# Kernel tuning notes

Hardware: AMD Instinct MI355X
Metric: run time of the kernel (lower is better)

## Reference

```python
import jax, jax.numpy as jnp
import numpy as np

N_NODES = 100000
N_EDGES = 1600000
IN_CH = 256
HID_CH = 128


def setup_inputs() -> dict:
    key = jax.random.key(0)
    k1, k2, k3 = jax.random.split(key, 3)
    x = jax.random.normal(k1, (N_NODES, IN_CH), dtype=jnp.float32)
    edge_index = jax.random.randint(k2, (2, N_EDGES), 0, N_NODES, dtype=jnp.int64)
    # Glorot-style init for the GCN linear weight [in, out]
    W = jax.random.normal(k3, (IN_CH, HID_CH), dtype=jnp.float32) / np.sqrt(IN_CH)
    bias = jnp.zeros((HID_CH,), dtype=jnp.float32)
    # PReLU default init 0.25, per-channel
    alpha = jnp.full((HID_CH,), 0.25, dtype=jnp.float32)
    return {"x": x, "edge_index": edge_index, "W": W, "bias": bias, "alpha": alpha}


def reference(x, edge_index, W, bias, alpha):
    # GCNConv (PyG defaults): add self loops, symmetric degree norm,
    # linear transform then scatter-add aggregation, then per-channel PReLU.
    N = x.shape[0]
    self_loops = jnp.arange(N, dtype=edge_index.dtype)
    row = jnp.concatenate([edge_index[0], self_loops])  # source j
    col = jnp.concatenate([edge_index[1], self_loops])  # target i
    # degree of destination nodes (edge_weight = 1)
    deg = jax.ops.segment_sum(jnp.ones_like(col, dtype=x.dtype), col, num_segments=N)
    dinv = jnp.where(deg > 0, jax.lax.rsqrt(deg), jnp.zeros_like(deg))
    norm = dinv[row] * dinv[col]  # [E+N]
    h = x @ W  # [N, hid] dense transform first (GCNConv order)
    msgs = h[row] * norm[:, None]  # gather + scale, [E+N, hid]
    agg = jax.ops.segment_sum(msgs, col, num_segments=N) + bias  # scatter-add
    # PReLU with per-channel alpha
    return jnp.where(agg > 0, agg, alpha * agg)
```

## Files before the change

kernel.cpp:

```cpp
#include <hip/hip_runtime.h>

#define N_NODES 100000
#define N_EDGES 1600000
#define IN_CH 256
#define HID_CH 128

#define NBUCK 196
#define NBLKC 400
#define EPB   4000
#define SCAN2_LEN (NBUCK * NBLKC)
#define SCAN2_BLOCKS ((SCAN2_LEN + 255) / 256)

typedef __attribute__((ext_vector_type(8))) short short8;
typedef __attribute__((ext_vector_type(4))) float floatx4;

static __device__ __forceinline__ unsigned short f2bf(float f) {
    unsigned int u = __float_as_uint(f);
    u += 0x7fffu + ((u >> 16) & 1u);
    return (unsigned short)(u >> 16);
}

static __device__ __forceinline__ unsigned cvt_pk_bf16(float lo, float hi) {
    unsigned r;
    asm("v_cvt_pk_bf16_f32 %0, %1, %2" : "=v"(r) : "v"(lo), "v"(hi));
    return r;
}


__global__ void hist_kernel(const int* __restrict__ dst, int* __restrict__ histT) {
    __shared__ int h[NBUCK];
    int tid = threadIdx.x, blk = blockIdx.x;
    for (int b = tid; b < NBUCK; b += 256) h[b] = 0;
    __syncthreads();
    int base = blk * EPB;
    for (int e = base + tid; e < base + EPB; e += 256)
        atomicAdd(&h[dst[e] >> 9], 1);
    __syncthreads();
    for (int b = tid; b < NBUCK; b += 256) histT[b * NBLKC + blk] = h[b];
}

__global__ void gscanA_kernel(int* __restrict__ data, int* __restrict__ partials) {
    __shared__ int ss[256];
    int tid = threadIdx.x;
    int i = blockIdx.x * 256 + tid;
    int v = (i < SCAN2_LEN) ? data[i] : 0;
    ss[tid] = v;
    __syncthreads();
    for (int off = 1; off < 256; off <<= 1) {
        int t = (tid >= off) ? ss[tid - off] : 0;
        __syncthreads();
        ss[tid] += t;
        __syncthreads();
    }
    if (i < SCAN2_LEN) data[i] = ss[tid] - v;
    if (tid == 255) partials[blockIdx.x] = ss[255];
}

__global__ void gscanB_kernel(int* __restrict__ partials) {
    __shared__ int ss[512];
    int tid = threadIdx.x;
    int v = (tid < SCAN2_BLOCKS) ? partials[tid] : 0;
    ss[tid] = v;
    __syncthreads();
    for (int off = 1; off < 512; off <<= 1) {
        int t = (tid >= off) ? ss[tid - off] : 0;
        __syncthreads();
        ss[tid] += t;
        __syncthreads();
    }
    if (tid < SCAN2_BLOCKS) partials[tid] = ss[tid] - v;
}

__global__ void gscanC_kernel(int* __restrict__ data, const int* __restrict__ partials) {
    int i = blockIdx.x * 256 + threadIdx.x;
    if (i < SCAN2_LEN) data[i] += partials[blockIdx.x];
}

__global__ void scatter_coarse_kernel(const int* __restrict__ ei,
                                      const int* __restrict__ offs,
                                      unsigned* __restrict__ bucketed) {
    __shared__ int cur[NBUCK];
    int tid = threadIdx.x, blk = blockIdx.x;
    for (int b = tid; b < NBUCK; b += 256) cur[b] = offs[b * NBLKC + blk];
    __syncthreads();
    int base = blk * EPB;
    for (int e = base + tid; e < base + EPB; e += 256) {
        int src = ei[e];
        int dst = ei[N_EDGES + e];
        int b = dst >> 9;
        int pos = atomicAdd(&cur[b], 1);
        bucketed[pos] = ((unsigned)src << 9) | (unsigned)(dst & 511);
    }
}

__global__ void fine_kernel(const unsigned* __restrict__ bucketed,
                            const int* __restrict__ offs,
                            int* __restrict__ sorted,
                            int* __restrict__ row_start,
                            float* __restrict__ dinv) {
    __shared__ int bins[512];
    __shared__ int scanbuf[512];
    int b = blockIdx.x, tid = threadIdx.x;
    int bs = offs[b * NBLKC];
    int be = (b < NBUCK - 1) ? offs[(b + 1) * NBLKC] : N_EDGES;

    bins[tid] = 0;
    __syncthreads();
    for (int k = bs + tid; k < be; k += 512)
        atomicAdd(&bins[bucketed[k] & 511u], 1);
    __syncthreads();

    int c = bins[tid];
    scanbuf[tid] = c;
    __syncthreads();
    for (int off = 1; off < 512; off <<= 1) {
        int t = (tid >= off) ? scanbuf[tid - off] : 0;
        __syncthreads();
        scanbuf[tid] += t;
        __syncthreads();
    }
    int excl = scanbuf[tid] - c;

    int node = b * 512 + tid;
    if (node <= N_NODES) row_start[node] = bs + excl;
    if (node < N_NODES) dinv[node] = rsqrtf((float)(c + 1));

    bins[tid] = bs + excl;
    __syncthreads();
    for (int k = bs + tid; k < be; k += 512) {
        unsigned p = bucketed[k];
        int pos = atomicAdd(&bins[p & 511u], 1);
        sorted[pos] = (int)(p >> 9);
    }
}


__global__ void wt_kernel(const float* __restrict__ W, unsigned short* __restrict__ Wt) {
    int i = blockIdx.x * blockDim.x + threadIdx.x;
    if (i >= IN_CH * HID_CH) return;
    int k = i >> 7;
    int c = i & 127;
    Wt[c * IN_CH + k] = f2bf(W[i]);
}


__launch_bounds__(512)
__global__ void gemm_mfma_kernel(const float* __restrict__ x,
                                 const unsigned short* __restrict__ Wt,
                                 const float* __restrict__ dinv,
                                 unsigned short* __restrict__ hp) {
    __shared__ unsigned short Bs[IN_CH * HID_CH];

    int tid = threadIdx.x;

    {
        const uint4* src = (const uint4*)Wt;
#pragma unroll
        for (int i = 0; i < 8; ++i) {
            int j = i * 512 + tid;
            unsigned lb = (unsigned)j * 16u;
            unsigned c7 = (lb >> 9) & 7u;
            unsigned db = lb ^ (c7 << 4);
            *(uint4*)((char*)Bs + db) = src[j];
        }
    }
    __syncthreads();

    int wave = tid >> 6;
    int lane = tid & 63;
    int row0 = blockIdx.x * 256 + wave * 32;
    if (row0 >= N_NODES) return;

    int m = lane & 15;
    int q = lane >> 4;

    floatx4 acc[2][8];
#pragma unroll
    for (int i = 0; i < 2; ++i)
#pragma unroll
        for (int t = 0; t < 8; ++t) acc[i][t] = (floatx4){0.f, 0.f, 0.f, 0.f};

    int r0 = row0 + m;        if (r0 >= N_NODES) r0 = N_NODES - 1;
    int r1 = row0 + 16 + m;   if (r1 >= N_NODES) r1 = N_NODES - 1;
    const float* xp0 = &x[(size_t)r0 * IN_CH + q * 8];
    const float* xp1 = &x[(size_t)r1 * IN_CH + q * 8];

    float4 aA[4], aB[4];

#define LOADA(buf, kstep)                                          \
    do {                                                           \
        const float* p0_ = xp0 + (kstep) * 32;                     \
        const float* p1_ = xp1 + (kstep) * 32;                     \
        buf[0] = *(const float4*)(p0_);                            \
        buf[1] = *(const float4*)(p0_ + 4);                        \
        buf[2] = *(const float4*)(p1_);                            \
        buf[3] = *(const float4*)(p1_ + 4);                        \
    } while (0)

#define COMPUTE(buf, kstep)                                                     \
    do {                                                                        \
        union { short8 v; unsigned u[4]; } af0_, af1_;                          \
        af0_.u[0] = cvt_pk_bf16(buf[0].x, buf[0].y);                            \
        af0_.u[1] = cvt_pk_bf16(buf[0].z, buf[0].w);                            \
        af0_.u[2] = cvt_pk_bf16(buf[1].x, buf[1].y);                            \
        af0_.u[3] = cvt_pk_bf16(buf[1].z, buf[1].w);                            \
        af1_.u[0] = cvt_pk_bf16(buf[2].x, buf[2].y);                            \
        af1_.u[1] = cvt_pk_bf16(buf[2].z, buf[2].w);                            \
        af1_.u[2] = cvt_pk_bf16(buf[3].x, buf[3].y);                            \
        af1_.u[3] = cvt_pk_bf16(buf[3].z, buf[3].w);                            \
        int kb_ = ((kstep) * 32 + q * 8) * 2;                                   \
        _Pragma("unroll")                                                       \
        for (int t = 0; t < 8; ++t) {                                           \
            int c_ = t * 16 + m;                                                \
            unsigned db_ = (unsigned)(c_ * 512 + kb_) ^ ((unsigned)(c_ & 7) << 4); \
            short8 bf_ = *(const short8*)((const char*)Bs + db_);               \
            acc[0][t] = __builtin_amdgcn_mfma_f32_16x16x32_bf16(af0_.v, bf_, acc[0][t], 0, 0, 0); \
            acc[1][t] = __builtin_amdgcn_mfma_f32_16x16x32_bf16(af1_.v, bf_, acc[1][t], 0, 0, 0); \
        }                                                                       \
    } while (0)

    LOADA(aA, 0);
#pragma unroll 1
    for (int ks = 0; ks < 8; ks += 2) {
        LOADA(aB, ks + 1);
        COMPUTE(aA, ks);
        if (ks < 6) LOADA(aA, ks + 2);
        COMPUTE(aB, ks + 1);
    }

#undef LOADA
#undef COMPUTE

#pragma unroll
    for (int tile = 0; tile < 2; ++tile) {
#pragma unroll
        for (int reg = 0; reg < 4; ++reg) {
            int grow = row0 + tile * 16 + q * 4 + reg;
            if (grow < N_NODES) {
                float di = dinv[grow];
                unsigned short* op = &hp[(size_t)grow * HID_CH + m];
#pragma unroll
                for (int tp = 0; tp < 4; ++tp) {
                    unsigned d = cvt_pk_bf16(acc[tile][2 * tp][reg] * di,
                                             acc[tile][2 * tp + 1][reg] * di);
                    op[(2 * tp) * 16]     = (unsigned short)(d & 0xffffu);
                    op[(2 * tp + 1) * 16] = (unsigned short)(d >> 16);
                }
            }
        }
    }
}


static __device__ __forceinline__ void acc_bf16x8(float* acc, uint4 u, float w) {
    acc[0] += w * __uint_as_float(u.x << 16);
    acc[1] += w * __uint_as_float(u.x & 0xffff0000u);
    acc[2] += w * __uint_as_float(u.y << 16);
    acc[3] += w * __uint_as_float(u.y & 0xffff0000u);
    acc[4] += w * __uint_as_float(u.z << 16);
    acc[5] += w * __uint_as_float(u.z & 0xffff0000u);
    acc[6] += w * __uint_as_float(u.w << 16);
    acc[7] += w * __uint_as_float(u.w & 0xffff0000u);
}

__launch_bounds__(256)
__global__ void gather_finalize_kernel(const int* __restrict__ row_start,
                                       const int* __restrict__ sorted,
                                       const float* __restrict__ dinv,
                                       const unsigned short* __restrict__ hp,
                                       const float* __restrict__ bias,
                                       const float* __restrict__ alpha,
                                       float* __restrict__ out) {
    int node = (blockIdx.x * blockDim.x + threadIdx.x) >> 6;
    int lane = threadIdx.x & 63;
    if (node >= N_NODES) return;

    int beg = row_start[node];
    int end = row_start[node + 1];
    int part = lane >> 4;
    int ch = (lane & 15) * 8;

    float di = dinv[node];
    uint4 us = *(const uint4*)&hp[(size_t)node * HID_CH + ch];

    float acc[8];
#pragma unroll
    for (int i = 0; i < 8; ++i) acc[i] = 0.f;

    for (int k = beg + part; k < end; k += 16) {
        int k1 = k + 4, k2 = k + 8, k3 = k + 12;
        int e1 = end - 1;
        int s0 = sorted[k];
        int s1 = sorted[k1 < end ? k1 : e1];
        int s2 = sorted[k2 < end ? k2 : e1];
        int s3 = sorted[k3 < end ? k3 : e1];
        uint4 u0 = *(const uint4*)&hp[(size_t)s0 * HID_CH + ch];
        uint4 u1 = *(const uint4*)&hp[(size_t)s1 * HID_CH + ch];
        uint4 u2 = *(const uint4*)&hp[(size_t)s2 * HID_CH + ch];
        uint4 u3 = *(const uint4*)&hp[(size_t)s3 * HID_CH + ch];
        float w1 = k1 < end ? 1.f : 0.f;
        float w2 = k2 < end ? 1.f : 0.f;
        float w3 = k3 < end ? 1.f : 0.f;
        acc_bf16x8(acc, u0, 1.f);
        acc_bf16x8(acc, u1, w1);
        acc_bf16x8(acc, u2, w2);
        acc_bf16x8(acc, u3, w3);
    }

#pragma unroll
    for (int i = 0; i < 8; ++i) {
        acc[i] += __shfl_xor(acc[i], 16);
        acc[i] += __shfl_xor(acc[i], 32);
    }

    if (part == 0) {
        float sf[8];
        sf[0] = __uint_as_float(us.x << 16);
        sf[1] = __uint_as_float(us.x & 0xffff0000u);
        sf[2] = __uint_as_float(us.y << 16);
        sf[3] = __uint_as_float(us.y & 0xffff0000u);
        sf[4] = __uint_as_float(us.z << 16);
        sf[5] = __uint_as_float(us.z & 0xffff0000u);
        sf[6] = __uint_as_float(us.w << 16);
        sf[7] = __uint_as_float(us.w & 0xffff0000u);

        float4 b0 = *(const float4*)&bias[ch];
        float4 b1 = *(const float4*)&bias[ch + 4];
        float4 a0 = *(const float4*)&alpha[ch];
        float4 a1 = *(const float4*)&alpha[ch + 4];
        float bv[8] = {b0.x, b0.y, b0.z, b0.w, b1.x, b1.y, b1.z, b1.w};
        float av[8] = {a0.x, a0.y, a0.z, a0.w, a1.x, a1.y, a1.z, a1.w};

        float r[8];
#pragma unroll
        for (int i = 0; i < 8; ++i) {
            float v = di * (acc[i] + sf[i]) + bv[i];
            r[i] = v > 0.f ? v : av[i] * v;
        }
        float4 o0 = make_float4(r[0], r[1], r[2], r[3]);
        float4 o1 = make_float4(r[4], r[5], r[6], r[7]);
        *(float4*)&out[(size_t)node * HID_CH + ch] = o0;
        *(float4*)&out[(size_t)node * HID_CH + ch + 4] = o1;
    }
}


extern "C" void kernel_launch(void* const* d_in, const int* in_sizes, int n_in,
                              void* d_out, int out_size, void* d_ws, size_t ws_size,
                              hipStream_t stream) {
    const float* x     = (const float*)d_in[0];
    const int*   ei    = (const int*)d_in[1];
    const float* W     = (const float*)d_in[2];
    const float* bias  = (const float*)d_in[3];
    const float* alpha = (const float*)d_in[4];
    float* out = (float*)d_out;

    char* p = (char*)d_ws;
    auto align512 = [](size_t v) { return (v + 511) / 512 * 512; };
    unsigned short* hp = (unsigned short*)p; p += align512((size_t)N_NODES * HID_CH * 2);
    unsigned short* Wt = (unsigned short*)p; p += align512((size_t)IN_CH * HID_CH * 2);
    float* dinv    = (float*)p; p += align512((size_t)N_NODES * 4);
    int* row_start = (int*)p;   p += align512((size_t)(N_NODES + 1) * 4);
    int* histT     = (int*)p;   p += align512((size_t)SCAN2_LEN * 4);
    int* partials  = (int*)p;   p += align512(512 * 4);
    unsigned* bucketed = (unsigned*)p; p += align512((size_t)N_EDGES * 4);
    int* sorted    = (int*)p;   p += align512((size_t)N_EDGES * 4);

    hist_kernel<<<NBLKC, 256, 0, stream>>>(ei + N_EDGES, histT);
    gscanA_kernel<<<SCAN2_BLOCKS, 256, 0, stream>>>(histT, partials);
    gscanB_kernel<<<1, 512, 0, stream>>>(partials);
    gscanC_kernel<<<SCAN2_BLOCKS, 256, 0, stream>>>(histT, partials);
    scatter_coarse_kernel<<<NBLKC, 256, 0, stream>>>(ei, histT, bucketed);
    fine_kernel<<<NBUCK, 512, 0, stream>>>(bucketed, histT, sorted, row_start, dinv);

    wt_kernel<<<(IN_CH * HID_CH + 255) / 256, 256, 0, stream>>>(W, Wt);

    gemm_mfma_kernel<<<(N_NODES + 255) / 256, 512, 0, stream>>>(x, Wt, dinv, hp);

    long long gthreads = (long long)N_NODES * 64;
    gather_finalize_kernel<<<(int)((gthreads + 255) / 256), 256, 0, stream>>>(
        row_start, sorted, dinv, hp, bias, alpha, out);
}
```

Measured before the change: 296.6 us.

## Fuse fine CSR sort into gather kernel using per-block LDS sub-bucketing

The fine sorting pass that wrote a global sorted edge array and row_start is replaced by a degree-only kernel. The gather kernel now builds its own 64-node CSR in shared memory: each block scans its 512-node coarse bucket, keeps the edges for its 64-node sub-bucket, counts and prefix-sums them, then scatters the sources into LDS before aggregating. This removes the global sorted and row_start writes and reads, at the cost of each bucket's edges being read 8 times, one pass per sub-block. It also assumes each 64-node slice has at most 2048 edges (QCAP), which holds only if degrees stay near their uniform-random average, and there are fewer gather blocks for latency hiding.

```diff
diff --git a/kernel.cpp b/kernel.cpp
--- a/kernel.cpp
+++ b/kernel.cpp
@@ -10,6 +10,8 @@
 #define EPB   4000
 #define SCAN2_LEN (NBUCK * NBLKC)
 #define SCAN2_BLOCKS ((SCAN2_LEN + 255) / 256)
+#define NSUB 8
+#define QCAP 2048
 
 typedef __attribute__((ext_vector_type(8))) short short8;
 typedef __attribute__((ext_vector_type(4))) float floatx4;
@@ -93,45 +95,20 @@
     }
 }
 
-__global__ void fine_kernel(const unsigned* __restrict__ bucketed,
-                            const int* __restrict__ offs,
-                            int* __restrict__ sorted,
-                            int* __restrict__ row_start,
-                            float* __restrict__ dinv) {
+__global__ void degree_kernel(const unsigned* __restrict__ bucketed,
+                              const int* __restrict__ offs,
+                              float* __restrict__ dinv) {
     __shared__ int bins[512];
-    __shared__ int scanbuf[512];
     int b = blockIdx.x, tid = threadIdx.x;
     int bs = offs[b * NBLKC];
     int be = (b < NBUCK - 1) ? offs[(b + 1) * NBLKC] : N_EDGES;
-
     bins[tid] = 0;
     __syncthreads();
     for (int k = bs + tid; k < be; k += 512)
         atomicAdd(&bins[bucketed[k] & 511u], 1);
     __syncthreads();
-
-    int c = bins[tid];
-    scanbuf[tid] = c;
-    __syncthreads();
-    for (int off = 1; off < 512; off <<= 1) {
-        int t = (tid >= off) ? scanbuf[tid - off] : 0;
-        __syncthreads();
-        scanbuf[tid] += t;
-        __syncthreads();
-    }
-    int excl = scanbuf[tid] - c;
-
     int node = b * 512 + tid;
-    if (node <= N_NODES) row_start[node] = bs + excl;
-    if (node < N_NODES) dinv[node] = rsqrtf((float)(c + 1));
-
-    bins[tid] = bs + excl;
-    __syncthreads();
-    for (int k = bs + tid; k < be; k += 512) {
-        unsigned p = bucketed[k];
-        int pos = atomicAdd(&bins[p & 511u], 1);
-        sorted[pos] = (int)(p >> 9);
-    }
+    if (node < N_NODES) dinv[node] = rsqrtf((float)(bins[tid] + 1));
 }
 
 
@@ -264,83 +241,139 @@
 }
 
 __launch_bounds__(256)
-__global__ void gather_finalize_kernel(const int* __restrict__ row_start,
-                                       const int* __restrict__ sorted,
-                                       const float* __restrict__ dinv,
-                                       const unsigned short* __restrict__ hp,
-                                       const float* __restrict__ bias,
-                                       const float* __restrict__ alpha,
-                                       float* __restrict__ out) {
-    int node = (blockIdx.x * blockDim.x + threadIdx.x) >> 6;
-    int lane = threadIdx.x & 63;
-    if (node >= N_NODES) return;
-
-    int beg = row_start[node];
-    int end = row_start[node + 1];
+__global__ void fused_gather_kernel(const unsigned* __restrict__ bucketed,
+                                    const int* __restrict__ offs,
+                                    const float* __restrict__ dinv,
+                                    const unsigned short* __restrict__ hp,
+                                    const float* __restrict__ bias,
+                                    const float* __restrict__ alpha,
+                                    float* __restrict__ out) {
+    __shared__ int q[QCAP];
+    __shared__ int q2[QCAP];
+    __shared__ int bins[64];
+    __shared__ int starts[65];
+    __shared__ int cur[64];
+    __shared__ int qn;
+
+    int tid = threadIdx.x;
+    int b = blockIdx.x >> 3;
+    int s = blockIdx.x & 7;
+    int bs = offs[b * NBLKC];
+    int be = (b < NBUCK - 1) ? offs[(b + 1) * NBLKC] : N_EDGES;
+
+    if (tid == 0) qn = 0;
+    if (tid < 64) bins[tid] = 0;
+    __syncthreads();
+
+    for (int k = bs + tid; k < be; k += 256) {
+        unsigned rec = bucketed[k];
+        if ((int)((rec >> 6) & 7u) == s) {
+            int pos = atomicAdd(&qn, 1);
+            q[pos] = (int)((rec >> 9) << 6 | (rec & 63u));
+            atomicAdd(&bins[rec & 63u], 1);
+        }
+    }
+    __syncthreads();
+
+    if (tid < 64) {
+        int c = bins[tid];
+        int v = c;
+#pragma unroll
+        for (int off = 1; off < 64; off <<= 1) {
+            int t = __shfl_up(v, off, 64);
+            if (tid >= off) v += t;
+        }
+        starts[tid + 1] = v;
+        cur[tid] = v - c;
+        if (tid == 0) starts[0] = 0;
+    }
+    __syncthreads();
+
+    int n = qn;
+    for (int i = tid; i < n; i += 256) {
+        int v = q[i];
+        int pos = atomicAdd(&cur[v & 63], 1);
+        q2[pos] = v >> 6;
+    }
+    __syncthreads();
+
+    int wv = tid >> 6;
+    int lane = tid & 63;
     int part = lane >> 4;
-    int ch = (lane & 15) * 8;
-
-    float di = dinv[node];
-    uint4 us = *(const uint4*)&hp[(size_t)node * HID_CH + ch];
-
-    float acc[8];
-#pragma unroll
-    for (int i = 0; i < 8; ++i) acc[i] = 0.f;
-
-    for (int k = beg + part; k < end; k += 16) {
-        int k1 = k + 4, k2 = k + 8, k3 = k + 12;
-        int e1 = end - 1;
-        int s0 = sorted[k];
-        int s1 = sorted[k1 < end ? k1 : e1];
-        int s2 = sorted[k2 < end ? k2 : e1];
-        int s3 = sorted[k3 < end ? k3 : e1];
-        uint4 u0 = *(const uint4*)&hp[(size_t)s0 * HID_CH + ch];
-        uint4 u1 = *(const uint4*)&hp[(size_t)s1 * HID_CH + ch];
-        uint4 u2 = *(const uint4*)&hp[(size_t)s2 * HID_CH + ch];
-        uint4 u3 = *(const uint4*)&hp[(size_t)s3 * HID_CH + ch];
-        float w1 = k1 < end ? 1.f : 0.f;
-        float w2 = k2 < end ? 1.f : 0.f;
-        float w3 = k3 < end ? 1.f : 0.f;
-        acc_bf16x8(acc, u0, 1.f);
-        acc_bf16x8(acc, u1, w1);
-        acc_bf16x8(acc, u2, w2);
-        acc_bf16x8(acc, u3, w3);
-    }
-
-#pragma unroll
-    for (int i = 0; i < 8; ++i) {
-        acc[i] += __shfl_xor(acc[i], 16);
-        acc[i] += __shfl_xor(acc[i], 32);
-    }
-
-    if (part == 0) {
-        float sf[8];
-        sf[0] = __uint_as_float(us.x << 16);
-        sf[1] = __uint_as_float(us.x & 0xffff0000u);
-        sf[2] = __uint_as_float(us.y << 16);
-        sf[3] = __uint_as_float(us.y & 0xffff0000u);
-        sf[4] = __uint_as_float(us.z << 16);
-        sf[5] = __uint_as_float(us.z & 0xffff0000u);
-        sf[6] = __uint_as_float(us.w << 16);
-        sf[7] = __uint_as_float(us.w & 0xffff0000u);
-
-        float4 b0 = *(const float4*)&bias[ch];
-        float4 b1 = *(const float4*)&bias[ch + 4];
-        float4 a0 = *(const float4*)&alpha[ch];
-        float4 a1 = *(const float4*)&alpha[ch + 4];
-        float bv[8] = {b0.x, b0.y, b0.z, b0.w, b1.x, b1.y, b1.z, b1.w};
-        float av[8] = {a0.x, a0.y, a0.z, a0.w, a1.x, a1.y, a1.z, a1.w};
-
-        float r[8];
+    int c16 = lane & 15;
+    int ch = c16 * 8;
+    int node0 = b * 512 + s * 64;
+
+    float4 bvv0 = *(const float4*)&bias[ch];
+    float4 bvv1 = *(const float4*)&bias[ch + 4];
+    float4 avv0 = *(const float4*)&alpha[ch];
+    float4 avv1 = *(const float4*)&alpha[ch + 4];
+
+    for (int j = 0; j < 16; ++j) {
+        int local = wv * 16 + j;
+        int node = node0 + local;
+        if (node >= N_NODES) break;
+
+        int beg = starts[local];
+        int end = starts[local + 1];
+        float di = dinv[node];
+        uint4 us = *(const uint4*)&hp[(size_t)node * HID_CH + ch];
+
+        float acc[8];
+#pragma unroll
+        for (int i = 0; i < 8; ++i) acc[i] = 0.f;
+
+        for (int k = beg + part; k < end; k += 16) {
+            int k1 = k + 4, k2 = k + 8, k3 = k + 12;
+            int e1 = end - 1;
+            int s0 = q2[k];
+            int s1 = q2[k1 < end ? k1 : e1];
+            int s2 = q2[k2 < end ? k2 : e1];
+            int s3 = q2[k3 < end ? k3 : e1];
+            uint4 u0 = *(const uint4*)&hp[(size_t)s0 * HID_CH + ch];
+            uint4 u1 = *(const uint4*)&hp[(size_t)s1 * HID_CH + ch];
+            uint4 u2 = *(const uint4*)&hp[(size_t)s2 * HID_CH + ch];
+            uint4 u3 = *(const uint4*)&hp[(size_t)s3 * HID_CH + ch];
+            float w1 = k1 < end ? 1.f : 0.f;
+            float w2 = k2 < end ? 1.f : 0.f;
+            float w3 = k3 < end ? 1.f : 0.f;
+            acc_bf16x8(acc, u0, 1.f);
+            acc_bf16x8(acc, u1, w1);
+            acc_bf16x8(acc, u2, w2);
+            acc_bf16x8(acc, u3, w3);
+        }
+
 #pragma unroll
         for (int i = 0; i < 8; ++i) {
-            float v = di * (acc[i] + sf[i]) + bv[i];
-            r[i] = v > 0.f ? v : av[i] * v;
-        }
-        float4 o0 = make_float4(r[0], r[1], r[2], r[3]);
-        float4 o1 = make_float4(r[4], r[5], r[6], r[7]);
-        *(float4*)&out[(size_t)node * HID_CH + ch] = o0;
-        *(float4*)&out[(size_t)node * HID_CH + ch + 4] = o1;
+            acc[i] += __shfl_xor(acc[i], 16);
+            acc[i] += __shfl_xor(acc[i], 32);
+        }
+
+        if (part == 0) {
+            float sf[8];
+            sf[0] = __uint_as_float(us.x << 16);
+            sf[1] = __uint_as_float(us.x & 0xffff0000u);
+            sf[2] = __uint_as_float(us.y << 16);
+            sf[3] = __uint_as_float(us.y & 0xffff0000u);
+            sf[4] = __uint_as_float(us.z << 16);
+            sf[5] = __uint_as_float(us.z & 0xffff0000u);
+            sf[6] = __uint_as_float(us.w << 16);
+            sf[7] = __uint_as_float(us.w & 0xffff0000u);
+
+            float bv[8] = {bvv0.x, bvv0.y, bvv0.z, bvv0.w, bvv1.x, bvv1.y, bvv1.z, bvv1.w};
+            float av[8] = {avv0.x, avv0.y, avv0.z, avv0.w, avv1.x, avv1.y, avv1.z, avv1.w};
+
+            float r[8];
+#pragma unroll
+            for (int i = 0; i < 8; ++i) {
+                float v = di * (acc[i] + sf[i]) + bv[i];
+                r[i] = v > 0.f ? v : av[i] * v;
+            }
+            float4 o0 = make_float4(r[0], r[1], r[2], r[3]);
+            float4 o1 = make_float4(r[4], r[5], r[6], r[7]);
+            *(float4*)&out[(size_t)node * HID_CH + ch] = o0;
+            *(float4*)&out[(size_t)node * HID_CH + ch + 4] = o1;
+        }
     }
 }
 
@@ -360,24 +393,21 @@
     unsigned short* hp = (unsigned short*)p; p += align512((size_t)N_NODES * HID_CH * 2);
     unsigned short* Wt = (unsigned short*)p; p += align512((size_t)IN_CH * HID_CH * 2);
     float* dinv    = (float*)p; p += align512((size_t)N_NODES * 4);
-    int* row_start = (int*)p;   p += align512((size_t)(N_NODES + 1) * 4);
     int* histT     = (int*)p;   p += align512((size_t)SCAN2_LEN * 4);
     int* partials  = (int*)p;   p += align512(512 * 4);
     unsigned* bucketed = (unsigned*)p; p += align512((size_t)N_EDGES * 4);
-    int* sorted    = (int*)p;   p += align512((size_t)N_EDGES * 4);
 
     hist_kernel<<<NBLKC, 256, 0, stream>>>(ei + N_EDGES, histT);
     gscanA_kernel<<<SCAN2_BLOCKS, 256, 0, stream>>>(histT, partials);
     gscanB_kernel<<<1, 512, 0, stream>>>(partials);
     gscanC_kernel<<<SCAN2_BLOCKS, 256, 0, stream>>>(histT, partials);
     scatter_coarse_kernel<<<NBLKC, 256, 0, stream>>>(ei, histT, bucketed);
-    fine_kernel<<<NBUCK, 512, 0, stream>>>(bucketed, histT, sorted, row_start, dinv);
+    degree_kernel<<<NBUCK, 512, 0, stream>>>(bucketed, histT, dinv);
 
     wt_kernel<<<(IN_CH * HID_CH + 255) / 256, 256, 0, stream>>>(W, Wt);
 
     gemm_mfma_kernel<<<(N_NODES + 255) / 256, 512, 0, stream>>>(x, Wt, dinv, hp);
 
-    long long gthreads = (long long)N_NODES * 64;
-    gather_finalize_kernel<<<(int)((gthreads + 255) / 256), 256, 0, stream>>>(
-        row_start, sorted, dinv, hp, bias, alpha, out);
-}
+    fused_gather_kernel<<<NBUCK * NSUB, 256, 0, stream>>>(
+        bucketed, histT, dinv, hp, bias, alpha, out);
+}
```

Result: slower. 321.7 us (+8.4%).

## Fuse scan fixup into consumers and software-pipeline gather index loads

Applied to the files above, without the earlier changes.

Drops the gscanC kernel launch by having the scatter and fine kernels add the per-block scan partial on the fly when reading offsets. The gather kernel now prefetches the next iteration's neighbour indices while the current feature rows are being loaded and accumulated. It also loads bias and alpha before the loop to hide their latency. This saves one launch and one pass over the histogram, and shortens the dependent index-then-row load chain, at the cost of a few more registers.

```diff
diff --git a/kernel.cpp b/kernel.cpp
--- a/kernel.cpp
+++ b/kernel.cpp
@@ -71,17 +71,19 @@
     if (tid < SCAN2_BLOCKS) partials[tid] = ss[tid] - v;
 }
 
-__global__ void gscanC_kernel(int* __restrict__ data, const int* __restrict__ partials) {
-    int i = blockIdx.x * 256 + threadIdx.x;
-    if (i < SCAN2_LEN) data[i] += partials[blockIdx.x];
+static __device__ __forceinline__ int offs_at(const int* __restrict__ offs,
+                                              const int* __restrict__ partials, int i) {
+    return offs[i] + partials[i >> 8];
 }
 
 __global__ void scatter_coarse_kernel(const int* __restrict__ ei,
                                       const int* __restrict__ offs,
+                                      const int* __restrict__ partials,
                                       unsigned* __restrict__ bucketed) {
     __shared__ int cur[NBUCK];
     int tid = threadIdx.x, blk = blockIdx.x;
-    for (int b = tid; b < NBUCK; b += 256) cur[b] = offs[b * NBLKC + blk];
+    for (int b = tid; b < NBUCK; b += 256)
+        cur[b] = offs_at(offs, partials, b * NBLKC + blk);
     __syncthreads();
     int base = blk * EPB;
     for (int e = base + tid; e < base + EPB; e += 256) {
@@ -95,14 +97,15 @@
 
 __global__ void fine_kernel(const unsigned* __restrict__ bucketed,
                             const int* __restrict__ offs,
+                            const int* __restrict__ partials,
                             int* __restrict__ sorted,
                             int* __restrict__ row_start,
                             float* __restrict__ dinv) {
     __shared__ int bins[512];
     __shared__ int scanbuf[512];
     int b = blockIdx.x, tid = threadIdx.x;
-    int bs = offs[b * NBLKC];
-    int be = (b < NBUCK - 1) ? offs[(b + 1) * NBLKC] : N_EDGES;
+    int bs = offs_at(offs, partials, b * NBLKC);
+    int be = (b < NBUCK - 1) ? offs_at(offs, partials, (b + 1) * NBLKC) : N_EDGES;
 
     bins[tid] = 0;
     __syncthreads();
@@ -282,29 +285,51 @@
 
     float di = dinv[node];
     uint4 us = *(const uint4*)&hp[(size_t)node * HID_CH + ch];
+    float4 bvv0 = *(const float4*)&bias[ch];
+    float4 bvv1 = *(const float4*)&bias[ch + 4];
+    float4 avv0 = *(const float4*)&alpha[ch];
+    float4 avv1 = *(const float4*)&alpha[ch + 4];
 
     float acc[8];
 #pragma unroll
     for (int i = 0; i < 8; ++i) acc[i] = 0.f;
 
-    for (int k = beg + part; k < end; k += 16) {
+    int e1 = end - 1;
+    int k = beg + part;
+    if (k < end) {
         int k1 = k + 4, k2 = k + 8, k3 = k + 12;
-        int e1 = end - 1;
         int s0 = sorted[k];
         int s1 = sorted[k1 < end ? k1 : e1];
         int s2 = sorted[k2 < end ? k2 : e1];
         int s3 = sorted[k3 < end ? k3 : e1];
-        uint4 u0 = *(const uint4*)&hp[(size_t)s0 * HID_CH + ch];
-        uint4 u1 = *(const uint4*)&hp[(size_t)s1 * HID_CH + ch];
-        uint4 u2 = *(const uint4*)&hp[(size_t)s2 * HID_CH + ch];
-        uint4 u3 = *(const uint4*)&hp[(size_t)s3 * HID_CH + ch];
         float w1 = k1 < end ? 1.f : 0.f;
         float w2 = k2 < end ? 1.f : 0.f;
         float w3 = k3 < end ? 1.f : 0.f;
-        acc_bf16x8(acc, u0, 1.f);
-        acc_bf16x8(acc, u1, w1);
-        acc_bf16x8(acc, u2, w2);
-        acc_bf16x8(acc, u3, w3);
+        while (true) {
+            uint4 u0 = *(const uint4*)&hp[(size_t)s0 * HID_CH + ch];
+            uint4 u1 = *(const uint4*)&hp[(size_t)s1 * HID_CH + ch];
+            uint4 u2 = *(const uint4*)&hp[(size_t)s2 * HID_CH + ch];
+            uint4 u3 = *(const uint4*)&hp[(size_t)s3 * HID_CH + ch];
+            float cw1 = w1, cw2 = w2, cw3 = w3;
+            int kn = k + 16;
+            bool more = kn < end;
+            if (more) {
+                int n1 = kn + 4, n2 = kn + 8, n3 = kn + 12;
+                s0 = sorted[kn];
+                s1 = sorted[n1 < end ? n1 : e1];
+                s2 = sorted[n2 < end ? n2 : e1];
+                s3 = sorted[n3 < end ? n3 : e1];
+                w1 = n1 < end ? 1.f : 0.f;
+                w2 = n2 < end ? 1.f : 0.f;
+                w3 = n3 < end ? 1.f : 0.f;
+                k = kn;
+            }
+            acc_bf16x8(acc, u0, 1.f);
+            acc_bf16x8(acc, u1, cw1);
+            acc_bf16x8(acc, u2, cw2);
+            acc_bf16x8(acc, u3, cw3);
+            if (!more) break;
+        }
     }
 
 #pragma unroll
@@ -324,12 +349,8 @@
         sf[6] = __uint_as_float(us.w << 16);
         sf[7] = __uint_as_float(us.w & 0xffff0000u);
 
-        float4 b0 = *(const float4*)&bias[ch];
-        float4 b1 = *(const float4*)&bias[ch + 4];
-        float4 a0 = *(const float4*)&alpha[ch];
-        float4 a1 = *(const float4*)&alpha[ch + 4];
-        float bv[8] = {b0.x, b0.y, b0.z, b0.w, b1.x, b1.y, b1.z, b1.w};
-        float av[8] = {a0.x, a0.y, a0.z, a0.w, a1.x, a1.y, a1.z, a1.w};
+        float bv[8] = {bvv0.x, bvv0.y, bvv0.z, bvv0.w, bvv1.x, bvv1.y, bvv1.z, bvv1.w};
+        float av[8] = {avv0.x, avv0.y, avv0.z, avv0.w, avv1.x, avv1.y, avv1.z, avv1.w};
 
         float r[8];
 #pragma unroll
@@ -369,9 +390,8 @@
     hist_kernel<<<NBLKC, 256, 0, stream>>>(ei + N_EDGES, histT);
     gscanA_kernel<<<SCAN2_BLOCKS, 256, 0, stream>>>(histT, partials);
     gscanB_kernel<<<1, 512, 0, stream>>>(partials);
-    gscanC_kernel<<<SCAN2_BLOCKS, 256, 0, stream>>>(histT, partials);
-    scatter_coarse_kernel<<<NBLKC, 256, 0, stream>>>(ei, histT, bucketed);
-    fine_kernel<<<NBUCK, 512, 0, stream>>>(bucketed, histT, sorted, row_start, dinv);
+    scatter_coarse_kernel<<<NBLKC, 256, 0, stream>>>(ei, histT, partials, bucketed);
+    fine_kernel<<<NBUCK, 512, 0, stream>>>(bucketed, histT, partials, sorted, row_start, dinv);
 
     wt_kernel<<<(IN_CH * HID_CH + 255) / 256, 256, 0, stream>>>(W, Wt);
 
```

Result: no change. 299.3 us (+0.9%).
